# Performance work log

Measured on AMD Instinct MI355X. Metric: run time of the kernel, lower is better.

## Reference

```python
import math
import jax, jax.numpy as jnp
import numpy as np

N_USERS = 100000
M_ITEMS = 50000
N_NODES = N_USERS + M_ITEMS
LATENT_DIM = 64
CLOCK_DIM = 64
N_CATS = 1000
N_LAYERS = 3
TIME_BINS = 24
TOPK = 3
NNZ = 4800000
BATCH = 1024
ALPHA = 0.5
MU = 0.0
SIGMA = 1.0
PADDING_IDX = 0


def setup_inputs() -> dict:
    key = jax.random.key(0)
    ks = jax.random.split(key, 10)
    user_emb = 0.1 * jax.random.normal(ks[0], (N_USERS, LATENT_DIM), dtype=jnp.float32)
    item_emb = 0.1 * jax.random.normal(ks[1], (M_ITEMS, LATENT_DIM), dtype=jnp.float32)
    cat_emb = 0.1 * jax.random.normal(ks[2], (N_CATS, CLOCK_DIM), dtype=jnp.float32)
    cat_emb = cat_emb.at[PADDING_IDX].set(0.0)  # padding_idx row zeroed
    graph_vals = jax.random.uniform(ks[3], (NNZ,), dtype=jnp.float32) / 32.0  # ~normalized adjacency values
    graph_rows = jax.random.randint(ks[4], (NNZ,), 0, N_NODES, dtype=jnp.int32)
    graph_cols = jax.random.randint(ks[5], (NNZ,), 0, N_NODES, dtype=jnp.int32)
    user_hour_top3 = jax.random.randint(ks[6], (N_USERS, TIME_BINS, TOPK), 0, N_CATS, dtype=jnp.int32)
    item_cat_ids = jax.random.randint(ks[7], (M_ITEMS,), 0, N_CATS, dtype=jnp.int32)
    users = jax.random.randint(ks[8], (BATCH,), 0, N_USERS, dtype=jnp.int32)
    thetas = jax.random.uniform(ks[9], (BATCH,), dtype=jnp.float32) * (2.0 * math.pi)
    return {"user_emb": user_emb, "item_emb": item_emb, "cat_emb": cat_emb,
            "graph_vals": graph_vals, "graph_rows": graph_rows, "graph_cols": graph_cols,
            "user_hour_top3": user_hour_top3, "item_cat_ids": item_cat_ids,
            "users": users, "thetas": thetas}


def _computer(user_emb, item_emb, graph_vals, graph_rows, graph_cols):
    # LightGCN propagation: sparse.mm applied n_layers times, then layer-mean.
    all_emb = jnp.concatenate([user_emb, item_emb], axis=0)  # [N, D]
    acc = all_emb
    e = all_emb
    for _ in range(N_LAYERS):
        msg = graph_vals[:, None] * e[graph_cols]             # [nnz, D]
        e = jax.ops.segment_sum(msg, graph_rows, num_segments=N_NODES)
        acc = acc + e
    light = acc / jnp.float32(N_LAYERS + 1)
    return light[:N_USERS], light[N_USERS:]


def _gaussian_hour_weights(thetas):
    cur = (thetas / (2.0 * math.pi) * TIME_BINS)[:, None]     # [B, 1]
    bins = jnp.arange(TIME_BINS, dtype=jnp.float32)[None, :]  # [1, 24]
    diff = jnp.abs(cur - bins)
    delta = jnp.minimum(diff, TIME_BINS - diff)                # circular distance
    w = jnp.exp(-jnp.square(delta - MU) / (2.0 * SIGMA * SIGMA))
    return w / (jnp.sum(w, axis=1, keepdims=True) + 1e-8)


def reference(user_emb, item_emb, cat_emb, graph_vals, graph_rows, graph_cols,
              user_hour_top3, item_cat_ids, users, thetas):
    all_users, all_items = _computer(user_emb, item_emb, graph_vals, graph_rows, graph_cols)
    u_emb = all_users[users]                                   # [B, D]
    base_scores = u_emb @ all_items.T                          # [B, M]
    # interest clock embedding
    top3 = user_hour_top3[users]                               # [B, 24, 3]
    hour_emb = cat_emb[top3].mean(axis=2)                      # [B, 24, Dc]
    weights = _gaussian_hour_weights(thetas)                   # [B, 24]
    v_clock = jnp.einsum('bh,bhd->bd', weights, hour_emb)      # [B, Dc]
    clock_scores = v_clock @ cat_emb[item_cat_ids].T           # [B, M]
    return base_scores + ALPHA * clock_scores
```

## Files before the change

kernel.cpp:

```cpp
#include <hip/hip_runtime.h>
#include <math.h>

#define N_USERS 100000
#define M_ITEMS 50000
#define N_NODES 150000
#define DIM 64
#define TIME_BINS 24
#define NNZ_CNT 4800000
#define BATCH 1024
#define NE (N_NODES * DIM)
#define NU (N_USERS * DIM)
#define NI (M_ITEMS * DIM)
#define TWO_PI 6.283185307179586f

#define BSHIFT 10
#define NB ((N_NODES + (1 << BSHIFT) - 1) >> BSHIFT)
#define CHUNK 4096
#define NCHUNKS ((NNZ_CNT + CHUNK - 1) / CHUNK)

#define SCB 1024
#define NSB ((N_NODES + SCB - 1) / SCB)

__global__ __launch_bounds__(256) void init_kernel(
    const float* __restrict__ user_emb, const float* __restrict__ item_emb,
    float* __restrict__ A, float* __restrict__ ACCI) {
  const int nA4 = NE / 4, nI4 = NI / 4, u4 = NU / 4;
  int stride = gridDim.x * blockDim.x;
  for (int i = blockIdx.x * blockDim.x + threadIdx.x; i < nA4 + nI4; i += stride) {
    if (i < nA4) {
      float4 v = (i < u4) ? ((const float4*)user_emb)[i]
                          : ((const float4*)item_emb)[i - u4];
      ((float4*)A)[i] = v;
    } else {
      ((float4*)ACCI)[i - nA4] = ((const float4*)item_emb)[i - nA4];
    }
  }
}

__global__ __launch_bounds__(256) void zero_kernel(int* __restrict__ p, int n) {
  int stride = gridDim.x * blockDim.x;
  for (int i = blockIdx.x * blockDim.x + threadIdx.x; i < n; i += stride)
    p[i] = 0;
}

__global__ __launch_bounds__(256) void hist_kernel(
    const int* __restrict__ rows, int* __restrict__ cnt) {
  int stride = gridDim.x * blockDim.x;
  for (int i = blockIdx.x * blockDim.x + threadIdx.x; i < NNZ_CNT; i += stride)
    atomicAdd(&cnt[rows[i]], 1);
}

__global__ __launch_bounds__(SCB) void scan_sums_kernel(
    const int* __restrict__ cnt, int* __restrict__ bsum) {
  int i = blockIdx.x * SCB + threadIdx.x;
  int x = (i < N_NODES) ? cnt[i] : 0;
#pragma unroll
  for (int off = 1; off < 64; off <<= 1) x += __shfl_xor(x, off);
  __shared__ int ws[SCB / 64];
  int wid = threadIdx.x >> 6, lane = threadIdx.x & 63;
  if (lane == 0) ws[wid] = x;
  __syncthreads();
  if (threadIdx.x == 0) {
    int s = 0;
#pragma unroll
    for (int w = 0; w < SCB / 64; ++w) s += ws[w];
    bsum[blockIdx.x] = s;
  }
}

__global__ __launch_bounds__(256) void scan_offsets_kernel(
    const int* __restrict__ bsum, int* __restrict__ boff, int* __restrict__ rp) {
  __shared__ int tmp[256];
  int t = threadIdx.x;
  int x = (t < NSB) ? bsum[t] : 0;
  tmp[t] = x;
  __syncthreads();
  for (int off = 1; off < 256; off <<= 1) {
    int y = (t >= off) ? tmp[t - off] : 0;
    __syncthreads();
    tmp[t] += y;
    __syncthreads();
  }
  if (t < NSB) boff[t] = tmp[t] - x;
  if (t == 255) rp[N_NODES] = tmp[255];
}

__global__ __launch_bounds__(SCB) void scan_write_kernel(
    const int* __restrict__ cnt, const int* __restrict__ boff,
    int* __restrict__ rp, int* __restrict__ cursor) {
  int i = blockIdx.x * SCB + threadIdx.x;
  int x = (i < N_NODES) ? cnt[i] : 0;
  int lane = threadIdx.x & 63, wid = threadIdx.x >> 6;
  int inc = x;
#pragma unroll
  for (int off = 1; off < 64; off <<= 1) {
    int y = __shfl_up(inc, off);
    if (lane >= off) inc += y;
  }
  __shared__ int ws[SCB / 64];
  if (lane == 63) ws[wid] = inc;
  __syncthreads();
  int wofs = 0;
  for (int w = 0; w < wid; ++w) wofs += ws[w];
  int excl = boff[blockIdx.x] + wofs + inc - x;
  if (i < N_NODES) {
    rp[i] = excl;
    cursor[i] = excl;
  }
}

__global__ __launch_bounds__(256) void binit_kernel(
    const int* __restrict__ rp, int* __restrict__ bcur) {
  int b = blockIdx.x * 256 + threadIdx.x;
  if (b < NB) bcur[b] = rp[b << BSHIFT];
}

__global__ __launch_bounds__(256) void bucket_stage_kernel(
    const int* __restrict__ rows, const int* __restrict__ cols,
    const float* __restrict__ vals, int* __restrict__ bcur,
    int2* __restrict__ stage) {
  __shared__ int lhist[NB];
  __shared__ int loffs[NB];
  __shared__ int gbase[NB];
  __shared__ int tmp[256];
  __shared__ int2 sitems[CHUNK];
  __shared__ unsigned char sbkt[CHUNK];

  const int tid = threadIdx.x;
  const int chunk0 = blockIdx.x * CHUNK;
  int n = NNZ_CNT - chunk0;
  if (n > CHUNK) n = CHUNK;

  for (int i = tid; i < NB; i += 256) lhist[i] = 0;
  __syncthreads();

  int key[16], vbits[16], pr[16];
#pragma unroll
  for (int u = 0; u < 16; ++u) {
    int li = u * 256 + tid;
    if (li < n) {
      int i = chunk0 + li;
      int r = rows[i];
      int c = cols[i];
      float v = vals[i];
      int b = r >> BSHIFT;
      int rank = atomicAdd(&lhist[b], 1);
      key[u] = ((r & ((1 << BSHIFT) - 1)) << 18) | c;
      vbits[u] = __float_as_int(v);
      pr[u] = (b << 12) | rank;
    } else {
      pr[u] = -1;
    }
  }
  __syncthreads();

  int x = (tid < NB) ? lhist[tid] : 0;
  tmp[tid] = x;
  __syncthreads();
  for (int off = 1; off < 256; off <<= 1) {
    int y = (tid >= off) ? tmp[tid - off] : 0;
    __syncthreads();
    tmp[tid] += y;
    __syncthreads();
  }
  if (tid < NB) {
    loffs[tid] = tmp[tid] - x;
    gbase[tid] = (x > 0) ? atomicAdd(&bcur[tid], x) : 0;
  }
  __syncthreads();

#pragma unroll
  for (int u = 0; u < 16; ++u) {
    if (pr[u] >= 0) {
      int b = pr[u] >> 12;
      int rank = pr[u] & 4095;
      int p = loffs[b] + rank;
      sitems[p] = make_int2(key[u], vbits[u]);
      sbkt[p] = (unsigned char)b;
    }
  }
  __syncthreads();

  for (int j = tid; j < n; j += 256) {
    int b = sbkt[j];
    int2 it = sitems[j];
    stage[gbase[b] + (j - loffs[b])] = it;
  }
}

__global__ __launch_bounds__(512) void bucket_scatter_kernel(
    const int2* __restrict__ stage, const int* __restrict__ rp,
    int* __restrict__ cursor, int2* __restrict__ pairs) {
  const int b = blockIdx.x;
  const int rbase = b << BSHIFT;
  int rend = rbase + (1 << BSHIFT);
  if (rend > N_NODES) rend = N_NODES;
  const int wstart = rp[rbase];
  const int wend = rp[rend];
  for (int j = wstart + threadIdx.x; j < wend; j += 512) {
    int2 it = stage[j];
    int r = rbase + (it.x >> 18);
    int c = it.x & 0x3FFFF;
    int pos = atomicAdd(&cursor[r], 1);
    pairs[pos] = make_int2(c, it.y);
  }
}

__global__ __launch_bounds__(256) void spmm_csr_kernel(
    const float* __restrict__ ecur, float* __restrict__ enext,
    float* __restrict__ ACCI, const int* __restrict__ rp,
    const int2* __restrict__ pairs) {
  int r = blockIdx.x * 4 + (threadIdx.x >> 6);
  int lane = threadIdx.x & 63;
  if (r >= N_NODES) return;
  int start = rp[r];
  int end = rp[r + 1];
  float acc = 0.f;

  for (int jb = start; jb < end; jb += 64) {
    int n = end - jb;
    if (n > 64) n = 64;
    int jj = jb + lane;
    if (jj >= end) jj = end - 1;
    int2 mp = pairs[jj];

    int k = 0;
    for (; k + 8 <= n; k += 8) {
      float v[8], g[8];
#pragma unroll
      for (int u = 0; u < 8; ++u) {
        int c = __shfl(mp.x, k + u);
        v[u] = __int_as_float(__shfl(mp.y, k + u));
        g[u] = ecur[c * DIM + lane];
      }
#pragma unroll
      for (int u = 0; u < 8; ++u) acc = fmaf(v[u], g[u], acc);
    }
    if (k + 4 <= n) {
      float v[4], g[4];
#pragma unroll
      for (int u = 0; u < 4; ++u) {
        int c = __shfl(mp.x, k + u);
        v[u] = __int_as_float(__shfl(mp.y, k + u));
        g[u] = ecur[c * DIM + lane];
      }
#pragma unroll
      for (int u = 0; u < 4; ++u) acc = fmaf(v[u], g[u], acc);
      k += 4;
    }
    for (; k < n; ++k) {
      int c = __shfl(mp.x, k);
      float v = __int_as_float(__shfl(mp.y, k));
      acc = fmaf(v, ecur[c * DIM + lane], acc);
    }
  }

  enext[r * DIM + lane] = acc;
  if (r >= N_USERS) {
    int ir = r - N_USERS;
    ACCI[ir * DIM + lane] += acc;
  }
}

__global__ __launch_bounds__(256) void uacc_kernel(
    const float* __restrict__ src, const int* __restrict__ users,
    float* __restrict__ UACC, int add) {
  int idx = blockIdx.x * 256 + threadIdx.x;
  int b = idx >> 6, d = idx & 63;
  int u = users[b];
  float v = src[u * DIM + d];
  if (add) UACC[idx] += v; else UACC[idx] = v;
}

__global__ __launch_bounds__(64) void clock_kernel(
    const int* __restrict__ users, const float* __restrict__ thetas,
    const int* __restrict__ top3, const float* __restrict__ cat_emb,
    const float* __restrict__ UACC, float* __restrict__ U2T) {
  int b = blockIdx.x;
  int d = threadIdx.x;
  int u = users[b];
  float cur = thetas[b] * ((float)TIME_BINS / TWO_PI);

  float w[TIME_BINS];
  float S = 0.f;
#pragma unroll
  for (int h = 0; h < TIME_BINS; ++h) {
    float diff = fabsf(cur - (float)h);
    float delta = fminf(diff, (float)TIME_BINS - diff);
    float wh = expf(-0.5f * delta * delta);
    w[h] = wh;
    S += wh;
  }
  float inv = 1.f / (S + 1e-8f);

  float v = 0.f;
#pragma unroll
  for (int h = 0; h < TIME_BINS; ++h) {
    int base = u * (TIME_BINS * 3) + h * 3;
    int i0 = top3[base + 0];
    int i1 = top3[base + 1];
    int i2 = top3[base + 2];
    float he = (cat_emb[i0 * DIM + d] + cat_emb[i1 * DIM + d] +
                cat_emb[i2 * DIM + d]) * (1.f / 3.f);
    v += w[h] * he;
  }
  U2T[d * BATCH + b] = 0.25f * UACC[b * DIM + d];
  U2T[(DIM + d) * BATCH + b] = 0.5f * v * inv;
}

__global__ __launch_bounds__(64) void build_it_kernel(
    const float* __restrict__ ACCI, const float* __restrict__ cat_emb,
    const int* __restrict__ item_cat, float* __restrict__ IT) {
  int m = blockIdx.x * 64 + threadIdx.x;
  if (m >= M_ITEMS) return;
  int cid = item_cat[m];
#pragma unroll 4
  for (int k = 0; k < DIM; ++k) {
    IT[k * M_ITEMS + m] = 0.25f * ACCI[m * DIM + k];
    IT[(DIM + k) * M_ITEMS + m] = cat_emb[cid * DIM + k];
  }
}

#define GK 32
#define LDP 72
__global__ __launch_bounds__(256) void gemm_kernel(
    const float* __restrict__ U2T, const float* __restrict__ IT,
    float* __restrict__ out) {
  __shared__ float sU[GK][LDP];
  __shared__ float sI[GK][LDP];
  const int m0 = blockIdx.x * 64;
  const int b0 = blockIdx.y * 64;
  const int tid = threadIdx.x;
  const int tx = tid & 15;
  const int ty = tid >> 4;
  const bool full = (m0 + 64 <= M_ITEMS);

  float acc[4][4] = {};

  for (int k0 = 0; k0 < 2 * DIM; k0 += GK) {
    int linear = tid * 8;
    int kk = linear >> 6;
    int col = linear & 63;
    {
      const float* src = &U2T[(k0 + kk) * BATCH + b0 + col];
      *(float4*)&sU[kk][col] = *(const float4*)(src);
      *(float4*)&sU[kk][col + 4] = *(const float4*)(src + 4);
    }
    if (full) {
      const float* src = &IT[(k0 + kk) * M_ITEMS + m0 + col];
      *(float4*)&sI[kk][col] = *(const float4*)(src);
      *(float4*)&sI[kk][col + 4] = *(const float4*)(src + 4);
    } else {
#pragma unroll
      for (int j = 0; j < 8; ++j) {
        int m = m0 + col + j;
        sI[kk][col + j] = (m < M_ITEMS) ? IT[(k0 + kk) * M_ITEMS + m] : 0.f;
      }
    }
    __syncthreads();

#pragma unroll
    for (int k = 0; k < GK; ++k) {
      float4 uv = *(const float4*)&sU[k][ty * 4];
      float4 iv = *(const float4*)&sI[k][tx * 4];
      float ua[4] = {uv.x, uv.y, uv.z, uv.w};
      float ia[4] = {iv.x, iv.y, iv.z, iv.w};
#pragma unroll
      for (int bi = 0; bi < 4; ++bi)
#pragma unroll
        for (int mi = 0; mi < 4; ++mi)
          acc[bi][mi] = fmaf(ua[bi], ia[mi], acc[bi][mi]);
    }
    __syncthreads();
  }

#pragma unroll
  for (int bi = 0; bi < 4; ++bi) {
    int b = b0 + ty * 4 + bi;
    int m = m0 + tx * 4;
    if (full) {
      float4 v = make_float4(acc[bi][0], acc[bi][1], acc[bi][2], acc[bi][3]);
      *(float4*)&out[b * M_ITEMS + m] = v;
    } else {
#pragma unroll
      for (int mi = 0; mi < 4; ++mi)
        if (m + mi < M_ITEMS) out[b * M_ITEMS + m + mi] = acc[bi][mi];
    }
  }
}

extern "C" void kernel_launch(void* const* d_in, const int* in_sizes, int n_in,
                              void* d_out, int out_size, void* d_ws, size_t ws_size,
                              hipStream_t stream) {
  const float* user_emb   = (const float*)d_in[0];
  const float* item_emb   = (const float*)d_in[1];
  const float* cat_emb    = (const float*)d_in[2];
  const float* graph_vals = (const float*)d_in[3];
  const int*   graph_rows = (const int*)d_in[4];
  const int*   graph_cols = (const int*)d_in[5];
  const int*   top3       = (const int*)d_in[6];
  const int*   item_cat   = (const int*)d_in[7];
  const int*   users      = (const int*)d_in[8];
  const float* thetas     = (const float*)d_in[9];
  float* out = (float*)d_out;

  float* A      = (float*)d_ws;
  float* B      = A + NE;
  int2*  pairs  = (int2*)(B + NE);
  float* ACCI   = (float*)(pairs + NNZ_CNT);
  float* UACC   = ACCI + NI;
  int*   cnt    = (int*)(UACC + BATCH * DIM);
  int*   rp     = cnt + (N_NODES + 1);
  int*   cursor = rp + (N_NODES + 1);
  int*   bcur   = cursor + N_NODES;
  int*   bsum   = bcur + NB;
  int*   boff   = bsum + NSB;
  int2* stage = (int2*)B;
  float* IT  = A;
  float* U2T = A + 2 * DIM * M_ITEMS;

  init_kernel<<<2048, 256, 0, stream>>>(user_emb, item_emb, A, ACCI);
  zero_kernel<<<256, 256, 0, stream>>>(cnt, N_NODES + 1);
  hist_kernel<<<2048, 256, 0, stream>>>(graph_rows, cnt);
  scan_sums_kernel<<<NSB, SCB, 0, stream>>>(cnt, bsum);
  scan_offsets_kernel<<<1, 256, 0, stream>>>(bsum, boff, rp);
  scan_write_kernel<<<NSB, SCB, 0, stream>>>(cnt, boff, rp, cursor);
  binit_kernel<<<1, 256, 0, stream>>>(rp, bcur);
  bucket_stage_kernel<<<NCHUNKS, 256, 0, stream>>>(graph_rows, graph_cols,
                                                   graph_vals, bcur, stage);
  bucket_scatter_kernel<<<NB, 512, 0, stream>>>(stage, rp, cursor, pairs);
  uacc_kernel<<<BATCH * DIM / 256, 256, 0, stream>>>(user_emb, users, UACC, 0);

  float* cur = A;
  float* nxt = B;
  for (int l = 0; l < 3; ++l) {
    spmm_csr_kernel<<<(N_NODES + 3) / 4, 256, 0, stream>>>(cur, nxt, ACCI, rp,
                                                           pairs);
    uacc_kernel<<<BATCH * DIM / 256, 256, 0, stream>>>(nxt, users, UACC, 1);
    float* t = cur; cur = nxt; nxt = t;
  }

  clock_kernel<<<BATCH, 64, 0, stream>>>(users, thetas, top3, cat_emb, UACC, U2T);
  build_it_kernel<<<(M_ITEMS + 63) / 64, 64, 0, stream>>>(ACCI, cat_emb,
                                                          item_cat, IT);
  dim3 ggrid((M_ITEMS + 63) / 64, BATCH / 64);
  gemm_kernel<<<ggrid, 256, 0, stream>>>(U2T, IT, out);
}
```

Baseline: 1.354 ms.

## Build CSR via bucket-level histogram and in-block row scan; enlarge GEMM tiles

Replaces the per-row global histogram and three-kernel scan with a coarse per-bucket histogram done in shared memory, then finalizes row offsets inside each bucket block using a shared-memory histogram and scan. This removes millions of global atomics on row counters and several small launches, and turns the scatter cursor atomics into shared-memory atomics. Separately, the output GEMM tile grows from 64x64 to 128x128 with an 8x8 per-thread register tile, raising arithmetic intensity at the cost of more registers and lower occupancy. The bucket scan assumes NB fits in 256 threads and that each bucket's rows fit in one 1024-thread block.

```diff
diff --git a/kernel.cpp b/kernel.cpp
--- a/kernel.cpp
+++ b/kernel.cpp
@@ -17,9 +17,6 @@
 #define NB ((N_NODES + (1 << BSHIFT) - 1) >> BSHIFT)
 #define CHUNK 4096
 #define NCHUNKS ((NNZ_CNT + CHUNK - 1) / CHUNK)
-
-#define SCB 1024
-#define NSB ((N_NODES + SCB - 1) / SCB)
 
 __global__ __launch_bounds__(256) void init_kernel(
     const float* __restrict__ user_emb, const float* __restrict__ item_emb,
@@ -43,36 +40,27 @@
     p[i] = 0;
 }
 
-__global__ __launch_bounds__(256) void hist_kernel(
-    const int* __restrict__ rows, int* __restrict__ cnt) {
-  int stride = gridDim.x * blockDim.x;
-  for (int i = blockIdx.x * blockDim.x + threadIdx.x; i < NNZ_CNT; i += stride)
-    atomicAdd(&cnt[rows[i]], 1);
-}
-
-__global__ __launch_bounds__(SCB) void scan_sums_kernel(
-    const int* __restrict__ cnt, int* __restrict__ bsum) {
-  int i = blockIdx.x * SCB + threadIdx.x;
-  int x = (i < N_NODES) ? cnt[i] : 0;
-#pragma unroll
-  for (int off = 1; off < 64; off <<= 1) x += __shfl_xor(x, off);
-  __shared__ int ws[SCB / 64];
-  int wid = threadIdx.x >> 6, lane = threadIdx.x & 63;
-  if (lane == 0) ws[wid] = x;
-  __syncthreads();
-  if (threadIdx.x == 0) {
-    int s = 0;
-#pragma unroll
-    for (int w = 0; w < SCB / 64; ++w) s += ws[w];
-    bsum[blockIdx.x] = s;
-  }
-}
-
-__global__ __launch_bounds__(256) void scan_offsets_kernel(
-    const int* __restrict__ bsum, int* __restrict__ boff, int* __restrict__ rp) {
+__global__ __launch_bounds__(256) void bhist_kernel(
+    const int* __restrict__ rows, int* __restrict__ bcnt) {
+  __shared__ int lh[NB];
+  for (int i = threadIdx.x; i < NB; i += 256) lh[i] = 0;
+  __syncthreads();
+  int stride = gridDim.x * 256;
+  for (int i = blockIdx.x * 256 + threadIdx.x; i < NNZ_CNT; i += stride)
+    atomicAdd(&lh[rows[i] >> BSHIFT], 1);
+  __syncthreads();
+  for (int i = threadIdx.x; i < NB; i += 256) {
+    int v = lh[i];
+    if (v) atomicAdd(&bcnt[i], v);
+  }
+}
+
+__global__ __launch_bounds__(256) void bscan_kernel(
+    const int* __restrict__ bcnt, int* __restrict__ bbase,
+    int* __restrict__ bcur, int* __restrict__ rp) {
   __shared__ int tmp[256];
   int t = threadIdx.x;
-  int x = (t < NSB) ? bsum[t] : 0;
+  int x = (t < NB) ? bcnt[t] : 0;
   tmp[t] = x;
   __syncthreads();
   for (int off = 1; off < 256; off <<= 1) {
@@ -81,38 +69,15 @@
     tmp[t] += y;
     __syncthreads();
   }
-  if (t < NSB) boff[t] = tmp[t] - x;
-  if (t == 255) rp[N_NODES] = tmp[255];
-}
-
-__global__ __launch_bounds__(SCB) void scan_write_kernel(
-    const int* __restrict__ cnt, const int* __restrict__ boff,
-    int* __restrict__ rp, int* __restrict__ cursor) {
-  int i = blockIdx.x * SCB + threadIdx.x;
-  int x = (i < N_NODES) ? cnt[i] : 0;
-  int lane = threadIdx.x & 63, wid = threadIdx.x >> 6;
-  int inc = x;
-#pragma unroll
-  for (int off = 1; off < 64; off <<= 1) {
-    int y = __shfl_up(inc, off);
-    if (lane >= off) inc += y;
-  }
-  __shared__ int ws[SCB / 64];
-  if (lane == 63) ws[wid] = inc;
-  __syncthreads();
-  int wofs = 0;
-  for (int w = 0; w < wid; ++w) wofs += ws[w];
-  int excl = boff[blockIdx.x] + wofs + inc - x;
-  if (i < N_NODES) {
-    rp[i] = excl;
-    cursor[i] = excl;
-  }
-}
-
-__global__ __launch_bounds__(256) void binit_kernel(
-    const int* __restrict__ rp, int* __restrict__ bcur) {
-  int b = blockIdx.x * 256 + threadIdx.x;
-  if (b < NB) bcur[b] = rp[b << BSHIFT];
+  if (t < NB) {
+    int e = tmp[t] - x;
+    bbase[t] = e;
+    bcur[t] = e;
+  }
+  if (t == NB - 1) {
+    bbase[NB] = tmp[t];
+    rp[N_NODES] = tmp[t];
+  }
 }
 
 __global__ __launch_bounds__(256) void bucket_stage_kernel(
@@ -188,20 +153,47 @@
   }
 }
 
-__global__ __launch_bounds__(512) void bucket_scatter_kernel(
-    const int2* __restrict__ stage, const int* __restrict__ rp,
-    int* __restrict__ cursor, int2* __restrict__ pairs) {
+__global__ __launch_bounds__(1024) void bucket_finalize_kernel(
+    const int2* __restrict__ stage, const int* __restrict__ bbase,
+    int* __restrict__ rp, int2* __restrict__ pairs) {
+  __shared__ int lhist[1 << BSHIFT];
+  __shared__ int lcur[1 << BSHIFT];
+  __shared__ int ws[16];
   const int b = blockIdx.x;
+  const int t = threadIdx.x;
   const int rbase = b << BSHIFT;
-  int rend = rbase + (1 << BSHIFT);
-  if (rend > N_NODES) rend = N_NODES;
-  const int wstart = rp[rbase];
-  const int wend = rp[rend];
-  for (int j = wstart + threadIdx.x; j < wend; j += 512) {
+  const int wstart = bbase[b];
+  const int wend = bbase[b + 1];
+
+  lhist[t] = 0;
+  __syncthreads();
+
+  for (int j = wstart + t; j < wend; j += 1024)
+    atomicAdd(&lhist[stage[j].x >> 18], 1);
+  __syncthreads();
+
+  int x = lhist[t];
+  int lane = t & 63, wid = t >> 6;
+  int inc = x;
+#pragma unroll
+  for (int off = 1; off < 64; off <<= 1) {
+    int y = __shfl_up(inc, off);
+    if (lane >= off) inc += y;
+  }
+  if (lane == 63) ws[wid] = inc;
+  __syncthreads();
+  int wofs = 0;
+  for (int w = 0; w < wid; ++w) wofs += ws[w];
+  int excl = wstart + wofs + inc - x;
+  lcur[t] = excl;
+  if (rbase + t < N_NODES) rp[rbase + t] = excl;
+  __syncthreads();
+
+  for (int j = wstart + t; j < wend; j += 1024) {
     int2 it = stage[j];
-    int r = rbase + (it.x >> 18);
+    int lr = it.x >> 18;
     int c = it.x & 0x3FFFF;
-    int pos = atomicAdd(&cursor[r], 1);
+    int pos = atomicAdd(&lcur[lr], 1);
     pairs[pos] = make_int2(c, it.y);
   }
 }
@@ -322,69 +314,71 @@
 }
 
 #define GK 32
-#define LDP 72
+#define GM 128
+#define GB 128
+#define LDW 132
 __global__ __launch_bounds__(256) void gemm_kernel(
     const float* __restrict__ U2T, const float* __restrict__ IT,
     float* __restrict__ out) {
-  __shared__ float sU[GK][LDP];
-  __shared__ float sI[GK][LDP];
-  const int m0 = blockIdx.x * 64;
-  const int b0 = blockIdx.y * 64;
+  __shared__ float sU[GK][LDW];
+  __shared__ float sI[GK][LDW];
+  const int m0 = blockIdx.x * GM;
+  const int b0 = blockIdx.y * GB;
   const int tid = threadIdx.x;
   const int tx = tid & 15;
   const int ty = tid >> 4;
-  const bool full = (m0 + 64 <= M_ITEMS);
-
-  float acc[4][4] = {};
+  const bool full = (m0 + GM <= M_ITEMS);
+
+  float acc[8][8] = {};
 
   for (int k0 = 0; k0 < 2 * DIM; k0 += GK) {
-    int linear = tid * 8;
-    int kk = linear >> 6;
-    int col = linear & 63;
-    {
-      const float* src = &U2T[(k0 + kk) * BATCH + b0 + col];
-      *(float4*)&sU[kk][col] = *(const float4*)(src);
-      *(float4*)&sU[kk][col + 4] = *(const float4*)(src + 4);
-    }
-    if (full) {
-      const float* src = &IT[(k0 + kk) * M_ITEMS + m0 + col];
-      *(float4*)&sI[kk][col] = *(const float4*)(src);
-      *(float4*)&sI[kk][col + 4] = *(const float4*)(src + 4);
-    } else {
-#pragma unroll
-      for (int j = 0; j < 8; ++j) {
-        int m = m0 + col + j;
-        sI[kk][col + j] = (m < M_ITEMS) ? IT[(k0 + kk) * M_ITEMS + m] : 0.f;
+#pragma unroll
+    for (int i = 0; i < 4; ++i) {
+      int f = i * 256 + tid;
+      int kk = f >> 5;
+      int c4 = (f & 31) * 4;
+      *(float4*)&sU[kk][c4] = *(const float4*)&U2T[(k0 + kk) * BATCH + b0 + c4];
+      if (full || (m0 + c4 + 3 < M_ITEMS)) {
+        *(float4*)&sI[kk][c4] = *(const float4*)&IT[(k0 + kk) * M_ITEMS + m0 + c4];
+      } else {
+        *(float4*)&sI[kk][c4] = make_float4(0.f, 0.f, 0.f, 0.f);
       }
     }
     __syncthreads();
 
 #pragma unroll
     for (int k = 0; k < GK; ++k) {
-      float4 uv = *(const float4*)&sU[k][ty * 4];
-      float4 iv = *(const float4*)&sI[k][tx * 4];
-      float ua[4] = {uv.x, uv.y, uv.z, uv.w};
-      float ia[4] = {iv.x, iv.y, iv.z, iv.w};
-#pragma unroll
-      for (int bi = 0; bi < 4; ++bi)
-#pragma unroll
-        for (int mi = 0; mi < 4; ++mi)
-          acc[bi][mi] = fmaf(ua[bi], ia[mi], acc[bi][mi]);
-    }
-    __syncthreads();
-  }
-
-#pragma unroll
-  for (int bi = 0; bi < 4; ++bi) {
-    int b = b0 + ty * 4 + bi;
-    int m = m0 + tx * 4;
-    if (full) {
-      float4 v = make_float4(acc[bi][0], acc[bi][1], acc[bi][2], acc[bi][3]);
-      *(float4*)&out[b * M_ITEMS + m] = v;
-    } else {
-#pragma unroll
-      for (int mi = 0; mi < 4; ++mi)
-        if (m + mi < M_ITEMS) out[b * M_ITEMS + m + mi] = acc[bi][mi];
+      float4 u0 = *(const float4*)&sU[k][ty * 4];
+      float4 u1 = *(const float4*)&sU[k][64 + ty * 4];
+      float4 i0 = *(const float4*)&sI[k][tx * 4];
+      float4 i1 = *(const float4*)&sI[k][64 + tx * 4];
+      float ub[8] = {u0.x, u0.y, u0.z, u0.w, u1.x, u1.y, u1.z, u1.w};
+      float im[8] = {i0.x, i0.y, i0.z, i0.w, i1.x, i1.y, i1.z, i1.w};
+#pragma unroll
+      for (int bi = 0; bi < 8; ++bi)
+#pragma unroll
+        for (int mj = 0; mj < 8; ++mj)
+          acc[bi][mj] = fmaf(ub[bi], im[mj], acc[bi][mj]);
+    }
+    __syncthreads();
+  }
+
+#pragma unroll
+  for (int bh = 0; bh < 2; ++bh) {
+#pragma unroll
+    for (int i = 0; i < 4; ++i) {
+      int b = b0 + bh * 64 + ty * 4 + i;
+#pragma unroll
+      for (int mh = 0; mh < 2; ++mh) {
+        int m = m0 + mh * 64 + tx * 4;
+        if (m + 3 < M_ITEMS) {
+          float4 v = make_float4(acc[bh * 4 + i][mh * 4 + 0],
+                                 acc[bh * 4 + i][mh * 4 + 1],
+                                 acc[bh * 4 + i][mh * 4 + 2],
+                                 acc[bh * 4 + i][mh * 4 + 3]);
+          *(float4*)&out[b * M_ITEMS + m] = v;
+        }
+      }
     }
   }
 }
@@ -409,26 +403,21 @@
   int2*  pairs  = (int2*)(B + NE);
   float* ACCI   = (float*)(pairs + NNZ_CNT);
   float* UACC   = ACCI + NI;
-  int*   cnt    = (int*)(UACC + BATCH * DIM);
-  int*   rp     = cnt + (N_NODES + 1);
-  int*   cursor = rp + (N_NODES + 1);
-  int*   bcur   = cursor + N_NODES;
-  int*   bsum   = bcur + NB;
-  int*   boff   = bsum + NSB;
+  int*   rp     = (int*)(UACC + BATCH * DIM);
+  int*   bcnt   = rp + (N_NODES + 1);
+  int*   bbase  = bcnt + NB;
+  int*   bcur   = bbase + (NB + 1);
   int2* stage = (int2*)B;
   float* IT  = A;
   float* U2T = A + 2 * DIM * M_ITEMS;
 
   init_kernel<<<2048, 256, 0, stream>>>(user_emb, item_emb, A, ACCI);
-  zero_kernel<<<256, 256, 0, stream>>>(cnt, N_NODES + 1);
-  hist_kernel<<<2048, 256, 0, stream>>>(graph_rows, cnt);
-  scan_sums_kernel<<<NSB, SCB, 0, stream>>>(cnt, bsum);
-  scan_offsets_kernel<<<1, 256, 0, stream>>>(bsum, boff, rp);
-  scan_write_kernel<<<NSB, SCB, 0, stream>>>(cnt, boff, rp, cursor);
-  binit_kernel<<<1, 256, 0, stream>>>(rp, bcur);
+  zero_kernel<<<1, 256, 0, stream>>>(bcnt, NB);
+  bhist_kernel<<<1024, 256, 0, stream>>>(graph_rows, bcnt);
+  bscan_kernel<<<1, 256, 0, stream>>>(bcnt, bbase, bcur, rp);
   bucket_stage_kernel<<<NCHUNKS, 256, 0, stream>>>(graph_rows, graph_cols,
                                                    graph_vals, bcur, stage);
-  bucket_scatter_kernel<<<NB, 512, 0, stream>>>(stage, rp, cursor, pairs);
+  bucket_finalize_kernel<<<NB, 1024, 0, stream>>>(stage, bbase, rp, pairs);
   uacc_kernel<<<BATCH * DIM / 256, 256, 0, stream>>>(user_emb, users, UACC, 0);
 
   float* cur = A;
@@ -443,6 +432,6 @@
   clock_kernel<<<BATCH, 64, 0, stream>>>(users, thetas, top3, cat_emb, UACC, U2T);
   build_it_kernel<<<(M_ITEMS + 63) / 64, 64, 0, stream>>>(ACCI, cat_emb,
                                                           item_cat, IT);
-  dim3 ggrid((M_ITEMS + 63) / 64, BATCH / 64);
+  dim3 ggrid((M_ITEMS + GM - 1) / GM, BATCH / GB);
   gemm_kernel<<<ggrid, 256, 0, stream>>>(U2T, IT, out);
 }
```

Result: faster. 1.128 ms (-16.7%).
